# Performance work log

Hardware: AMD Instinct MI355X
Metric: run time of the kernel (lower is better)

The kernel has to match this reference:

```python
import jax, jax.numpy as jnp
import numpy as np

B, IN, H = 16384, 512, 1024

def setup_inputs() -> dict:
    key = jax.random.key(0)
    ks = jax.random.split(key, 9)
    s_h = 1.0 / np.sqrt(H)
    s_x = 1.0 / np.sqrt(IN)
    return {
        "x": jax.random.normal(ks[0], (B, IN), jnp.float32),
        "h_prev": jax.random.normal(ks[1], (B, H), jnp.float32),
        # SLIM1 gates: Linear(H->H, bias=True)
        "W_u": jax.random.uniform(ks[2], (H, H), jnp.float32, -s_h, s_h),
        "b_u": jax.random.uniform(ks[3], (H,), jnp.float32, -s_h, s_h),
        "W_r": jax.random.uniform(ks[4], (H, H), jnp.float32, -s_h, s_h),
        "b_r": jax.random.uniform(ks[5], (H,), jnp.float32, -s_h, s_h),
        # hidden candidate: Linear(IN->H, bias=False) and Linear(H->H, bias=True)
        "W_hx": jax.random.uniform(ks[6], (H, IN), jnp.float32, -s_x, s_x),
        "W_hh": jax.random.uniform(ks[7], (H, H), jnp.float32, -s_h, s_h),
        "b_h": jax.random.uniform(ks[8], (H,), jnp.float32, -s_h, s_h),
    }

def reference(x, h_prev, W_u, b_u, W_r, b_r, W_hx, W_hh, b_h):
    # update and reset gates depend only on h_prev (SLIM1: sigmoid(W h + b))
    u = jax.nn.sigmoid(h_prev @ W_u.T + b_u)          # [B, H]
    r = jax.nn.sigmoid(h_prev @ W_r.T + b_r)          # [B, H]
    # candidate hidden state: tanh(W_hx x + W_hh (r*h) + b)
    h_cand = jnp.tanh(x @ W_hx.T + (r * h_prev) @ W_hh.T + b_h)  # [B, H]
    h_next = (1.0 - u) * h_prev + u * h_cand
    return (h_next, h_next)
```

## Files before the change

kernel.cpp:

```cpp
#include <hip/hip_runtime.h>
#include <hip/hip_bf16.h>

#define M_DIM 16384
#define IN_DIM 512
#define H_DIM 1024
#define BH (M_DIM * H_DIM)
#define K2 1536

typedef float f32x4 __attribute__((ext_vector_type(4)));
typedef short bf16x8 __attribute__((ext_vector_type(8)));

static __device__ __forceinline__ unsigned short f2bf(float f) {
    union { float f; unsigned u; } a; a.f = f;
    unsigned r = a.u + 0x7fffu + ((a.u >> 16) & 1u);
    return (unsigned short)(r >> 16);
}
static __device__ __forceinline__ float bf2f(unsigned short u) {
    union { unsigned u; float f; } a; a.u = (unsigned)u << 16;
    return a.f;
}

#define OFF_HB   0u
#define OFF_A2   16777216u
#define OFF_WU   41943040u
#define OFF_WR   42991616u
#define OFF_W2   44040192u
#define OFF_U16  45613056u
#define WS2_ELEMS 62390272u
#define WS2_NEED_BYTES (WS2_ELEMS * 2ull)

__global__ __launch_bounds__(256) void k_conv(const float* __restrict__ x,
                                              const float* __restrict__ h,
                                              const float* __restrict__ wu,
                                              const float* __restrict__ whx,
                                              const float* __restrict__ whh,
                                              const float* __restrict__ wr,
                                              unsigned short* __restrict__ ws) {
    const int total = 3604480;
    for (int u = blockIdx.x * blockDim.x + threadIdx.x; u < total;
         u += gridDim.x * blockDim.x) {
        const float* src; unsigned short* d; int lu;
        if (u < 2097152)      { lu = u;
                                src = h + (size_t)lu * 8;
                                d = ws + OFF_HB + (size_t)lu * 8; }
        else if (u < 3145728) { lu = u - 2097152;
                                src = x + (size_t)lu * 8;
                                d = ws + OFF_A2 + (size_t)(lu >> 6) * K2 + (lu & 63) * 8; }
        else if (u < 3276800) { lu = u - 3145728;
                                src = wu + (size_t)lu * 8;
                                d = ws + OFF_WU + (size_t)lu * 8; }
        else if (u < 3342336) { lu = u - 3276800;
                                src = whx + (size_t)lu * 8;
                                d = ws + OFF_W2 + (size_t)(lu >> 6) * K2 + (lu & 63) * 8; }
        else if (u < 3473408) { lu = u - 3342336;
                                src = whh + (size_t)lu * 8;
                                d = ws + OFF_W2 + (size_t)(lu >> 7) * K2 + 512 + (lu & 127) * 8; }
        else                  { lu = u - 3473408;
                                src = wr + (size_t)lu * 8;
                                d = ws + OFF_WR + (size_t)lu * 8; }
        float4 a = *reinterpret_cast<const float4*>(src);
        float4 b = *reinterpret_cast<const float4*>(src + 4);
        uint4 p;
        p.x = (unsigned)f2bf(a.x) | ((unsigned)f2bf(a.y) << 16);
        p.y = (unsigned)f2bf(a.z) | ((unsigned)f2bf(a.w) << 16);
        p.z = (unsigned)f2bf(b.x) | ((unsigned)f2bf(b.y) << 16);
        p.w = (unsigned)f2bf(b.z) | ((unsigned)f2bf(b.w) << 16);
        *reinterpret_cast<uint4*>(d) = p;
    }
}

#define SLOT_E 24576

static __device__ __forceinline__ void stage_half512(const unsigned short* __restrict__ src,
                                                     int rowBase, int ld, int ks,
                                                     unsigned short* lds, int tid) {
#pragma unroll
    for (int i = 0; i < 2; ++i) {
        int c = i * 512 + tid;
        int r = c >> 3, kc = c & 7;
        int gc = kc ^ (r & 7);
        const unsigned short* g = src + (size_t)(rowBase + r) * ld + ks + gc * 8;
        __builtin_amdgcn_global_load_lds((const __attribute__((address_space(1))) void*)g,
                                         (__attribute__((address_space(3))) void*)(lds + c * 8),
                                         16, 0, 0);
    }
}

template <int NT>
static __device__ __forceinline__ void gemm_pipe(const unsigned short* __restrict__ A, int aLd,
                                                 const unsigned short* __restrict__ B, int bLd,
                                                 int bm, int bn, unsigned short* L,
                                                 int tid, int wm, int wn, int frow, int klane,
                                                 f32x4 acc[4][4]) {
    auto stage_unit = [&](int t, int u) {
        unsigned short* slot = L + (t % 3) * SLOT_E;
        if (u == 0)      stage_half512(A, bm * 256,       aLd, t * 64, slot,         tid);
        else if (u == 1) stage_half512(A, bm * 256 + 128, aLd, t * 64, slot + 8192,  tid);
        else             stage_half512(B, bn * 128,       bLd, t * 64, slot + 16384, tid);
    };

    stage_unit(0, 0); stage_unit(0, 1); stage_unit(0, 2);
    stage_unit(1, 0); stage_unit(1, 1); stage_unit(1, 2);
    asm volatile("s_waitcnt vmcnt(6)" ::: "memory");
    __builtin_amdgcn_s_barrier();

    for (int t = 0; t < NT; ++t) {
        const unsigned short* base  = L + (t % 3) * SLOT_E;
        const unsigned short* bbase = base + 16384;
        bf16x8 bv[4][2];
#pragma unroll
        for (int q = 0; q < 4; ++q) {
            if (q == 0) {
#pragma unroll
                for (int n = 0; n < 4; ++n)
#pragma unroll
                    for (int kk = 0; kk < 2; ++kk) {
                        int pr = wn * 64 + n * 16 + frow;
                        bv[n][kk] = *reinterpret_cast<const bf16x8*>(
                            &bbase[pr * 64 + (((kk << 2) + klane) ^ (pr & 7)) * 8]);
                    }
            }
            bf16x8 av[2];
#pragma unroll
            for (int kk = 0; kk < 2; ++kk) {
                int pr = wm * 64 + q * 16 + frow;
                av[kk] = *reinterpret_cast<const bf16x8*>(
                    &base[pr * 64 + (((kk << 2) + klane) ^ (pr & 7)) * 8]);
            }
            if (q < 3 && t + 2 < NT) stage_unit(t + 2, q);
            __builtin_amdgcn_s_barrier();
            __builtin_amdgcn_s_setprio(1);
#pragma unroll
            for (int kk = 0; kk < 2; ++kk)
#pragma unroll
                for (int n = 0; n < 4; ++n)
                    acc[q][n] = __builtin_amdgcn_mfma_f32_16x16x32_bf16(av[kk], bv[n][kk], acc[q][n], 0, 0, 0);
            __builtin_amdgcn_s_setprio(0);
            if (q < 3) __builtin_amdgcn_s_barrier();
        }
        if (t < NT - 2)       { asm volatile("s_waitcnt vmcnt(6)" ::: "memory"); }
        else if (t == NT - 2) { asm volatile("s_waitcnt vmcnt(0)" ::: "memory"); }
        __builtin_amdgcn_s_barrier();
    }
}

__global__ __launch_bounds__(512, 1) void k_rgate_s(const unsigned short* __restrict__ hb,
                                                    const unsigned short* __restrict__ wrb,
                                                    const float* __restrict__ b_r,
                                                    unsigned short* __restrict__ rhA2) {
    __shared__ unsigned short L[3 * SLOT_E];
    int bid = blockIdx.x;
    int swz = (bid & 7) * 64 + (bid >> 3);
    int bm = swz >> 3, bn = swz & 7;
    int tid = threadIdx.x;
    int wave = tid >> 6, lane = tid & 63;
    int wm = wave >> 1, wn = wave & 1;
    int frow = lane & 15, klane = lane >> 4;

    f32x4 acc[4][4] = {};
    gemm_pipe<16>(hb, H_DIM, wrb, H_DIM, bm, bn, L, tid, wm, wn, frow, klane, acc);

    int rbase = bm * 256 + wm * 64;
    int cbase = bn * 128 + wn * 64;
#pragma unroll
    for (int q = 0; q < 4; ++q) {
#pragma unroll
        for (int n = 0; n < 4; ++n) {
            int col = cbase + n * 16 + frow;
            float bs = b_r[col];
#pragma unroll
            for (int qq = 0; qq < 4; ++qq) {
                int row = rbase + q * 16 + klane * 4 + qq;
                float g = 1.0f / (1.0f + __expf(-(acc[q][n][qq] + bs)));
                rhA2[(size_t)row * K2 + col] = f2bf(g * bf2f(hb[(size_t)row * H_DIM + col]));
            }
        }
    }
}

__global__ __launch_bounds__(512, 1) void k_ugate_s(const unsigned short* __restrict__ hb,
                                                    const unsigned short* __restrict__ wub,
                                                    const float* __restrict__ b_u,
                                                    unsigned short* __restrict__ u16) {
    __shared__ unsigned short L[3 * SLOT_E];
    int bid = blockIdx.x;
    int swz = (bid & 7) * 64 + (bid >> 3);
    int bm = swz >> 3, bn = swz & 7;
    int tid = threadIdx.x;
    int wave = tid >> 6, lane = tid & 63;
    int wm = wave >> 1, wn = wave & 1;
    int frow = lane & 15, klane = lane >> 4;

    f32x4 acc[4][4] = {};
    gemm_pipe<16>(hb, H_DIM, wub, H_DIM, bm, bn, L, tid, wm, wn, frow, klane, acc);

    int rbase = bm * 256 + wm * 64;
    int cbase = bn * 128 + wn * 64;
#pragma unroll
    for (int q = 0; q < 4; ++q) {
#pragma unroll
        for (int n = 0; n < 4; ++n) {
            int col = cbase + n * 16 + frow;
            float bs = b_u[col];
#pragma unroll
            for (int qq = 0; qq < 4; ++qq) {
                int row = rbase + q * 16 + klane * 4 + qq;
                float g = 1.0f / (1.0f + __expf(-(acc[q][n][qq] + bs)));
                u16[(size_t)row * H_DIM + col] = f2bf(g);
            }
        }
    }
}

__global__ __launch_bounds__(512, 1) void k_cand_b(const unsigned short* __restrict__ a2,
                                                   const unsigned short* __restrict__ w2,
                                                   const unsigned short* __restrict__ hb,
                                                   const unsigned short* __restrict__ u16,
                                                   const float* __restrict__ b_h,
                                                   float* __restrict__ out) {
    __shared__ unsigned short L[3 * SLOT_E];
    int bid = blockIdx.x;
    int swz = (bid & 7) * 64 + (bid >> 3);
    int bm = swz >> 3, bn = swz & 7;
    int tid = threadIdx.x;
    int wave = tid >> 6, lane = tid & 63;
    int wm = wave >> 1, wn = wave & 1;
    int frow = lane & 15, klane = lane >> 4;

    f32x4 acc[4][4] = {};
    gemm_pipe<24>(a2, K2, w2, K2, bm, bn, L, tid, wm, wn, frow, klane, acc);

    int rbase = bm * 256 + wm * 64;
    int cbase = bn * 128 + wn * 64;
#pragma unroll
    for (int q = 0; q < 4; ++q) {
#pragma unroll
        for (int n = 0; n < 4; ++n) {
            int col = cbase + n * 16 + frow;
            float bh = b_h[col];
#pragma unroll
            for (int qq = 0; qq < 4; ++qq) {
                int row = rbase + q * 16 + klane * 4 + qq;
                size_t off = (size_t)row * H_DIM + col;
                float hp = bf2f(hb[off]);
                float u = bf2f(u16[off]);
                float cpre = acc[q][n][qq] + bh;
                cpre = fminf(fmaxf(cpre, -15.0f), 15.0f);
                float e = __expf(2.0f * cpre);
                float c = (e - 1.0f) / (e + 1.0f);
                float h = hp + u * (c - hp);
                out[off] = h;
                out[BH + off] = h;
            }
        }
    }
}

#define LDSS 40

static __device__ __forceinline__ void stage_f32(const float* __restrict__ src, int rowBase,
                                                 int ld, int kBase,
                                                 unsigned short* lds, int tid) {
#pragma unroll
    for (int i = 0; i < 4; ++i) {
        int idx = i * 256 + tid;
        int r = idx >> 3, c4 = idx & 7;
        const float4 v = *reinterpret_cast<const float4*>(
            src + (size_t)(rowBase + r) * ld + kBase + c4 * 4);
        uint2 p;
        p.x = (unsigned)f2bf(v.x) | ((unsigned)f2bf(v.y) << 16);
        p.y = (unsigned)f2bf(v.z) | ((unsigned)f2bf(v.w) << 16);
        *reinterpret_cast<uint2*>(lds + r * LDSS + c4 * 4) = p;
    }
}

static __device__ __forceinline__ void stage_bf16s(const unsigned short* __restrict__ src,
                                                   int rowBase, int ld, int kBase,
                                                   unsigned short* lds, int tid) {
#pragma unroll
    for (int i = 0; i < 2; ++i) {
        int idx = i * 256 + tid;
        int r = idx >> 2, c8 = idx & 3;
        const uint4 v = *reinterpret_cast<const uint4*>(
            src + (size_t)(rowBase + r) * ld + kBase + c8 * 8);
        *reinterpret_cast<uint4*>(lds + r * LDSS + c8 * 8) = v;
    }
}

__global__ __launch_bounds__(256, 2) void k_rgate(const float* __restrict__ h_prev,
                                                  const float* __restrict__ W_r,
                                                  const float* __restrict__ b_r,
                                                  unsigned short* __restrict__ rh) {
    __shared__ unsigned short As[128 * LDSS];
    __shared__ unsigned short Bs[128 * LDSS];
    int bid = blockIdx.x;
    int swz = (bid & 7) * 128 + (bid >> 3);
    int bm = swz >> 3, bn = swz & 7;
    int tid = threadIdx.x;
    int wave = tid >> 6, lane = tid & 63;
    int wm = wave >> 1, wn = wave & 1;
    int frow = lane & 15, koff = (lane >> 4) * 8;
    f32x4 acc[4][4] = {};
    for (int ks = 0; ks < H_DIM; ks += 32) {
        stage_f32(h_prev, bm * 128, H_DIM, ks, As, tid);
        stage_f32(W_r, bn * 128, H_DIM, ks, Bs, tid);
        __syncthreads();
        bf16x8 av[4], bv[4];
#pragma unroll
        for (int m = 0; m < 4; ++m)
            av[m] = *reinterpret_cast<const bf16x8*>(&As[(wm * 64 + m * 16 + frow) * LDSS + koff]);
#pragma unroll
        for (int n = 0; n < 4; ++n)
            bv[n] = *reinterpret_cast<const bf16x8*>(&Bs[(wn * 64 + n * 16 + frow) * LDSS + koff]);
#pragma unroll
        for (int m = 0; m < 4; ++m)
#pragma unroll
            for (int n = 0; n < 4; ++n)
                acc[m][n] = __builtin_amdgcn_mfma_f32_16x16x32_bf16(av[m], bv[n], acc[m][n], 0, 0, 0);
        __syncthreads();
    }
    int rbase = bm * 128 + wm * 64, cbase = bn * 128 + wn * 64;
#pragma unroll
    for (int m = 0; m < 4; ++m)
#pragma unroll
        for (int n = 0; n < 4; ++n) {
            int col = cbase + n * 16 + frow;
            float bias = b_r[col];
#pragma unroll
            for (int q = 0; q < 4; ++q) {
                int row = rbase + m * 16 + (lane >> 4) * 4 + q;
                float pre = acc[m][n][q] + bias;
                float rv = 1.0f / (1.0f + __expf(-pre));
                rh[(size_t)row * H_DIM + col] = f2bf(rv * h_prev[(size_t)row * H_DIM + col]);
            }
        }
}

__global__ __launch_bounds__(256, 2) void k_fused(const float* __restrict__ x,
                                                  const float* __restrict__ h_prev,
                                                  const float* __restrict__ W_u,
                                                  const float* __restrict__ b_u,
                                                  const float* __restrict__ W_hx,
                                                  const float* __restrict__ W_hh,
                                                  const float* __restrict__ b_h,
                                                  const unsigned short* __restrict__ rh,
                                                  float* __restrict__ out) {
    __shared__ unsigned short As[128 * LDSS];
    __shared__ unsigned short Bs[128 * LDSS];
    int bid = blockIdx.x;
    int swz = (bid & 7) * 128 + (bid >> 3);
    int bm = swz >> 3, bn = swz & 7;
    int tid = threadIdx.x;
    int wave = tid >> 6, lane = tid & 63;
    int wm = wave >> 1, wn = wave & 1;
    int frow = lane & 15, koff = (lane >> 4) * 8;
    f32x4 accu[4][4] = {};
    f32x4 accc[4][4] = {};
    for (int ks = 0; ks < H_DIM; ks += 32) {
        stage_f32(h_prev, bm * 128, H_DIM, ks, As, tid);
        stage_f32(W_u, bn * 128, H_DIM, ks, Bs, tid);
        __syncthreads();
        bf16x8 av[4], bv[4];
#pragma unroll
        for (int m = 0; m < 4; ++m)
            av[m] = *reinterpret_cast<const bf16x8*>(&As[(wm * 64 + m * 16 + frow) * LDSS + koff]);
#pragma unroll
        for (int n = 0; n < 4; ++n)
            bv[n] = *reinterpret_cast<const bf16x8*>(&Bs[(wn * 64 + n * 16 + frow) * LDSS + koff]);
#pragma unroll
        for (int m = 0; m < 4; ++m)
#pragma unroll
            for (int n = 0; n < 4; ++n)
                accu[m][n] = __builtin_amdgcn_mfma_f32_16x16x32_bf16(av[m], bv[n], accu[m][n], 0, 0, 0);
        __syncthreads();
    }
    for (int ks = 0; ks < IN_DIM; ks += 32) {
        stage_f32(x, bm * 128, IN_DIM, ks, As, tid);
        stage_f32(W_hx, bn * 128, IN_DIM, ks, Bs, tid);
        __syncthreads();
        bf16x8 av[4], bv[4];
#pragma unroll
        for (int m = 0; m < 4; ++m)
            av[m] = *reinterpret_cast<const bf16x8*>(&As[(wm * 64 + m * 16 + frow) * LDSS + koff]);
#pragma unroll
        for (int n = 0; n < 4; ++n)
            bv[n] = *reinterpret_cast<const bf16x8*>(&Bs[(wn * 64 + n * 16 + frow) * LDSS + koff]);
#pragma unroll
        for (int m = 0; m < 4; ++m)
#pragma unroll
            for (int n = 0; n < 4; ++n)
                accc[m][n] = __builtin_amdgcn_mfma_f32_16x16x32_bf16(av[m], bv[n], accc[m][n], 0, 0, 0);
        __syncthreads();
    }
    for (int ks = 0; ks < H_DIM; ks += 32) {
        stage_bf16s(rh, bm * 128, H_DIM, ks, As, tid);
        stage_f32(W_hh, bn * 128, H_DIM, ks, Bs, tid);
        __syncthreads();
        bf16x8 av[4], bv[4];
#pragma unroll
        for (int m = 0; m < 4; ++m)
            av[m] = *reinterpret_cast<const bf16x8*>(&As[(wm * 64 + m * 16 + frow) * LDSS + koff]);
#pragma unroll
        for (int n = 0; n < 4; ++n)
            bv[n] = *reinterpret_cast<const bf16x8*>(&Bs[(wn * 64 + n * 16 + frow) * LDSS + koff]);
#pragma unroll
        for (int m = 0; m < 4; ++m)
#pragma unroll
            for (int n = 0; n < 4; ++n)
                accc[m][n] = __builtin_amdgcn_mfma_f32_16x16x32_bf16(av[m], bv[n], accc[m][n], 0, 0, 0);
        __syncthreads();
    }
    int rbase = bm * 128 + wm * 64, cbase = bn * 128 + wn * 64;
#pragma unroll
    for (int m = 0; m < 4; ++m)
#pragma unroll
        for (int n = 0; n < 4; ++n) {
            int col = cbase + n * 16 + frow;
            float bu = b_u[col], bh = b_h[col];
#pragma unroll
            for (int q = 0; q < 4; ++q) {
                int row = rbase + m * 16 + (lane >> 4) * 4 + q;
                size_t off = (size_t)row * H_DIM + col;
                float hp = h_prev[off];
                float u = 1.0f / (1.0f + __expf(-(accu[m][n][q] + bu)));
                float cpre = accc[m][n][q] + bh;
                cpre = fminf(fmaxf(cpre, -15.0f), 15.0f);
                float e = __expf(2.0f * cpre);
                float c = (e - 1.0f) / (e + 1.0f);
                float h = hp + u * (c - hp);
                out[off] = h;
                out[BH + off] = h;
            }
        }
}

extern "C" void kernel_launch(void* const* d_in, const int* in_sizes, int n_in,
                              void* d_out, int out_size, void* d_ws, size_t ws_size,
                              hipStream_t stream) {
    const float* x      = (const float*)d_in[0];
    const float* h_prev = (const float*)d_in[1];
    const float* W_u    = (const float*)d_in[2];
    const float* b_u    = (const float*)d_in[3];
    const float* W_r    = (const float*)d_in[4];
    const float* b_r    = (const float*)d_in[5];
    const float* W_hx   = (const float*)d_in[6];
    const float* W_hh   = (const float*)d_in[7];
    const float* b_h    = (const float*)d_in[8];
    float* out = (float*)d_out;

    if (ws_size >= WS2_NEED_BYTES) {
        unsigned short* ws = (unsigned short*)d_ws;
        hipLaunchKernelGGL(k_conv, dim3(2048), dim3(256), 0, stream,
                           x, h_prev, W_u, W_hx, W_hh, W_r, ws);
        hipLaunchKernelGGL(k_rgate_s, dim3(512), dim3(512), 0, stream,
                           ws + OFF_HB, ws + OFF_WR, b_r, ws + OFF_A2 + 512);
        hipLaunchKernelGGL(k_ugate_s, dim3(512), dim3(512), 0, stream,
                           ws + OFF_HB, ws + OFF_WU, b_u, ws + OFF_U16);
        hipLaunchKernelGGL(k_cand_b, dim3(512), dim3(512), 0, stream,
                           ws + OFF_A2, ws + OFF_W2, ws + OFF_HB, ws + OFF_U16,
                           b_h, out);
    } else {
        unsigned short* rh = (unsigned short*)d_ws;
        hipLaunchKernelGGL(k_rgate, dim3(1024), dim3(256), 0, stream, h_prev, W_r, b_r, rh);
        hipLaunchKernelGGL(k_fused, dim3(1024), dim3(256), 0, stream,
                           x, h_prev, W_u, b_u, W_hx, W_hh, b_h, rh, out);
    }
}
```

Baseline: 209.9 us.

## Switch bf16 GEMMs to 256x256 tiles with double-buffered quadrant pipeline

Replaces the 256x128 block tile with a triple-buffered LDS pipeline by a 256x256 tile, with 8 waves in a 2x4 layout each holding a 128x64 accumulator. Staging is double-buffered and split into A/B halves that are prefetched between four MFMA quadrant phases. The grid is halved to 256 blocks for all three GEMM kernels. The aim is more arithmetic per byte loaded from global memory and LDS. In exchange, register pressure doubles for the accumulators, and with 256 blocks on a 256-CU part there is only one wave of work, so any imbalance is not hidden.

Result: no change. 207.2 us (-1.3%).

```diff
diff --git a/kernel.cpp b/kernel.cpp
--- a/kernel.cpp
+++ b/kernel.cpp
@@ -69,109 +69,130 @@
     }
 }
 
-#define SLOT_E 24576
-
-static __device__ __forceinline__ void stage_half512(const unsigned short* __restrict__ src,
-                                                     int rowBase, int ld, int ks,
-                                                     unsigned short* lds, int tid) {
-#pragma unroll
-    for (int i = 0; i < 2; ++i) {
-        int c = i * 512 + tid;
-        int r = c >> 3, kc = c & 7;
-        int gc = kc ^ (r & 7);
-        const unsigned short* g = src + (size_t)(rowBase + r) * ld + ks + gc * 8;
-        __builtin_amdgcn_global_load_lds((const __attribute__((address_space(1))) void*)g,
-                                         (__attribute__((address_space(3))) void*)(lds + c * 8),
-                                         16, 0, 0);
-    }
-}
-
 template <int NT>
-static __device__ __forceinline__ void gemm_pipe(const unsigned short* __restrict__ A, int aLd,
-                                                 const unsigned short* __restrict__ B, int bLd,
-                                                 int bm, int bn, unsigned short* L,
-                                                 int tid, int wm, int wn, int frow, int klane,
-                                                 f32x4 acc[4][4]) {
-    auto stage_unit = [&](int t, int u) {
-        unsigned short* slot = L + (t % 3) * SLOT_E;
-        if (u == 0)      stage_half512(A, bm * 256,       aLd, t * 64, slot,         tid);
-        else if (u == 1) stage_half512(A, bm * 256 + 128, aLd, t * 64, slot + 8192,  tid);
-        else             stage_half512(B, bn * 128,       bLd, t * 64, slot + 16384, tid);
+static __device__ __forceinline__ void gemm_256(const unsigned short* __restrict__ A, int aLd,
+                                                const unsigned short* __restrict__ B, int bLd,
+                                                int bm, int bn, unsigned short* L, int tid,
+                                                int wm, int wn, int frow, int klane,
+                                                f32x4 acc[8][4]) {
+    auto stA = [&](int t, int mh) {
+#pragma unroll
+        for (int i = 0; i < 2; ++i) {
+            int c = i * 512 + tid;
+            int rp = c >> 3, kc = c & 7;
+            int gc = kc ^ (rp & 7);
+            int grow = bm * 256 + mh * 64 + (rp & 63) + ((rp >> 6) << 7);
+            const unsigned short* g = A + (size_t)grow * aLd + t * 64 + gc * 8;
+            unsigned short* l = L + (t & 1) * 32768 + mh * 8192 + c * 8;
+            __builtin_amdgcn_global_load_lds((const __attribute__((address_space(1))) void*)g,
+                                             (__attribute__((address_space(3))) void*)l, 16, 0, 0);
+        }
     };
-
-    stage_unit(0, 0); stage_unit(0, 1); stage_unit(0, 2);
-    stage_unit(1, 0); stage_unit(1, 1); stage_unit(1, 2);
-    asm volatile("s_waitcnt vmcnt(6)" ::: "memory");
+    auto stB = [&](int t, int nh) {
+#pragma unroll
+        for (int i = 0; i < 2; ++i) {
+            int c = i * 512 + tid;
+            int rp = c >> 3, kc = c & 7;
+            int gc = kc ^ (rp & 7);
+            int grow = bn * 256 + nh * 32 + (rp & 31) + ((rp >> 5) << 6);
+            const unsigned short* g = B + (size_t)grow * bLd + t * 64 + gc * 8;
+            unsigned short* l = L + (t & 1) * 32768 + 16384 + nh * 8192 + c * 8;
+            __builtin_amdgcn_global_load_lds((const __attribute__((address_space(1))) void*)g,
+                                             (__attribute__((address_space(3))) void*)l, 16, 0, 0);
+        }
+    };
+
+    stA(0, 0); stA(0, 1); stB(0, 0); stB(0, 1);
+    stA(1, 0); stB(1, 0);
+    asm volatile("s_waitcnt vmcnt(4)" ::: "memory");
     __builtin_amdgcn_s_barrier();
 
-    for (int t = 0; t < NT; ++t) {
-        const unsigned short* base  = L + (t % 3) * SLOT_E;
-        const unsigned short* bbase = base + 16384;
-        bf16x8 bv[4][2];
-#pragma unroll
-        for (int q = 0; q < 4; ++q) {
-            if (q == 0) {
-#pragma unroll
-                for (int n = 0; n < 4; ++n)
-#pragma unroll
-                    for (int kk = 0; kk < 2; ++kk) {
-                        int pr = wn * 64 + n * 16 + frow;
-                        bv[n][kk] = *reinterpret_cast<const bf16x8*>(
-                            &bbase[pr * 64 + (((kk << 2) + klane) ^ (pr & 7)) * 8]);
-                    }
-            }
-            bf16x8 av[2];
-#pragma unroll
-            for (int kk = 0; kk < 2; ++kk) {
-                int pr = wm * 64 + q * 16 + frow;
-                av[kk] = *reinterpret_cast<const bf16x8*>(
-                    &base[pr * 64 + (((kk << 2) + klane) ^ (pr & 7)) * 8]);
-            }
-            if (q < 3 && t + 2 < NT) stage_unit(t + 2, q);
-            __builtin_amdgcn_s_barrier();
-            __builtin_amdgcn_s_setprio(1);
-#pragma unroll
-            for (int kk = 0; kk < 2; ++kk)
-#pragma unroll
-                for (int n = 0; n < 4; ++n)
-                    acc[q][n] = __builtin_amdgcn_mfma_f32_16x16x32_bf16(av[kk], bv[n][kk], acc[q][n], 0, 0, 0);
-            __builtin_amdgcn_s_setprio(0);
-            if (q < 3) __builtin_amdgcn_s_barrier();
-        }
-        if (t < NT - 2)       { asm volatile("s_waitcnt vmcnt(6)" ::: "memory"); }
-        else if (t == NT - 2) { asm volatile("s_waitcnt vmcnt(0)" ::: "memory"); }
-        __builtin_amdgcn_s_barrier();
-    }
+#define LOAD_AV(mh)                                                                  \
+    _Pragma("unroll") for (int mf = 0; mf < 4; ++mf)                                 \
+        _Pragma("unroll") for (int kk = 0; kk < 2; ++kk) {                           \
+            int rp = wm * 64 + mf * 16 + frow;                                       \
+            av[mf][kk] = *reinterpret_cast<const bf16x8*>(                           \
+                &Lb[(mh) * 8192 + rp * 64 + (((kk << 2) + klane) ^ (rp & 7)) * 8]);  \
+        }
+#define LOAD_BV(nh)                                                                  \
+    _Pragma("unroll") for (int nf = 0; nf < 2; ++nf)                                 \
+        _Pragma("unroll") for (int kk = 0; kk < 2; ++kk) {                           \
+            int rp = wn * 32 + nf * 16 + frow;                                       \
+            bv[nf][kk] = *reinterpret_cast<const bf16x8*>(                           \
+                &LbB[(nh) * 8192 + rp * 64 + (((kk << 2) + klane) ^ (rp & 7)) * 8]); \
+        }
+#define MFMA_Q(mbase, nbase)                                                         \
+    __builtin_amdgcn_s_setprio(1);                                                   \
+    _Pragma("unroll") for (int kk = 0; kk < 2; ++kk)                                 \
+        _Pragma("unroll") for (int mf = 0; mf < 4; ++mf)                             \
+            _Pragma("unroll") for (int nf = 0; nf < 2; ++nf)                         \
+                acc[(mbase) + mf][(nbase) + nf] =                                    \
+                    __builtin_amdgcn_mfma_f32_16x16x32_bf16(                         \
+                        av[mf][kk], bv[nf][kk], acc[(mbase) + mf][(nbase) + nf],     \
+                        0, 0, 0);                                                    \
+    __builtin_amdgcn_s_setprio(0);
+
+    for (int g = 0; g < NT; ++g) {
+        const unsigned short* Lb = L + (g & 1) * 32768;
+        const unsigned short* LbB = Lb + 16384;
+        bf16x8 av[4][2], bv[2][2];
+
+        LOAD_AV(0); LOAD_BV(0);
+        if (g + 1 < NT) stA(g + 1, 1);
+        __builtin_amdgcn_s_barrier();
+        MFMA_Q(0, 0);
+        __builtin_amdgcn_s_barrier();
+        LOAD_BV(1);
+        if (g + 1 < NT) stB(g + 1, 1);
+        __builtin_amdgcn_s_barrier();
+        MFMA_Q(0, 2);
+        __builtin_amdgcn_s_barrier();
+        LOAD_AV(1); LOAD_BV(0);
+        if (g + 2 < NT) stA(g + 2, 0);
+        __builtin_amdgcn_s_barrier();
+        MFMA_Q(4, 0);
+        __builtin_amdgcn_s_barrier();
+        LOAD_BV(1);
+        if (g + 2 < NT) stB(g + 2, 0);
+        __builtin_amdgcn_s_barrier();
+        MFMA_Q(4, 2);
+        if (g < NT - 2)       { asm volatile("s_waitcnt vmcnt(4)" ::: "memory"); }
+        else if (g == NT - 2) { asm volatile("s_waitcnt vmcnt(0)" ::: "memory"); }
+        __builtin_amdgcn_s_barrier();
+    }
+#undef LOAD_AV
+#undef LOAD_BV
+#undef MFMA_Q
 }
 
 __global__ __launch_bounds__(512, 1) void k_rgate_s(const unsigned short* __restrict__ hb,
                                                     const unsigned short* __restrict__ wrb,
                                                     const float* __restrict__ b_r,
                                                     unsigned short* __restrict__ rhA2) {
-    __shared__ unsigned short L[3 * SLOT_E];
+    __shared__ unsigned short L[65536];
     int bid = blockIdx.x;
-    int swz = (bid & 7) * 64 + (bid >> 3);
-    int bm = swz >> 3, bn = swz & 7;
+    int swz = (bid & 7) * 32 + (bid >> 3);
+    int bm = swz >> 2, bn = swz & 3;
     int tid = threadIdx.x;
     int wave = tid >> 6, lane = tid & 63;
-    int wm = wave >> 1, wn = wave & 1;
+    int wm = wave >> 2, wn = wave & 3;
     int frow = lane & 15, klane = lane >> 4;
 
-    f32x4 acc[4][4] = {};
-    gemm_pipe<16>(hb, H_DIM, wrb, H_DIM, bm, bn, L, tid, wm, wn, frow, klane, acc);
-
-    int rbase = bm * 256 + wm * 64;
-    int cbase = bn * 128 + wn * 64;
-#pragma unroll
-    for (int q = 0; q < 4; ++q) {
-#pragma unroll
-        for (int n = 0; n < 4; ++n) {
-            int col = cbase + n * 16 + frow;
+    f32x4 acc[8][4] = {};
+    gemm_256<16>(hb, H_DIM, wrb, H_DIM, bm, bn, L, tid, wm, wn, frow, klane, acc);
+
+    int rbase = bm * 256 + wm * 128;
+    int cbase = bn * 256 + wn * 64;
+#pragma unroll
+    for (int a = 0; a < 8; ++a) {
+#pragma unroll
+        for (int nn = 0; nn < 4; ++nn) {
+            int col = cbase + nn * 16 + frow;
             float bs = b_r[col];
 #pragma unroll
-            for (int qq = 0; qq < 4; ++qq) {
-                int row = rbase + q * 16 + klane * 4 + qq;
-                float g = 1.0f / (1.0f + __expf(-(acc[q][n][qq] + bs)));
+            for (int q = 0; q < 4; ++q) {
+                int row = rbase + a * 16 + klane * 4 + q;
+                float g = 1.0f / (1.0f + __expf(-(acc[a][nn][q] + bs)));
                 rhA2[(size_t)row * K2 + col] = f2bf(g * bf2f(hb[(size_t)row * H_DIM + col]));
             }
         }
@@ -182,30 +203,30 @@
                                                     const unsigned short* __restrict__ wub,
                                                     const float* __restrict__ b_u,
                                                     unsigned short* __restrict__ u16) {
-    __shared__ unsigned short L[3 * SLOT_E];
+    __shared__ unsigned short L[65536];
     int bid = blockIdx.x;
-    int swz = (bid & 7) * 64 + (bid >> 3);
-    int bm = swz >> 3, bn = swz & 7;
+    int swz = (bid & 7) * 32 + (bid >> 3);
+    int bm = swz >> 2, bn = swz & 3;
     int tid = threadIdx.x;
     int wave = tid >> 6, lane = tid & 63;
-    int wm = wave >> 1, wn = wave & 1;
+    int wm = wave >> 2, wn = wave & 3;
     int frow = lane & 15, klane = lane >> 4;
 
-    f32x4 acc[4][4] = {};
-    gemm_pipe<16>(hb, H_DIM, wub, H_DIM, bm, bn, L, tid, wm, wn, frow, klane, acc);
-
-    int rbase = bm * 256 + wm * 64;
-    int cbase = bn * 128 + wn * 64;
-#pragma unroll
-    for (int q = 0; q < 4; ++q) {
-#pragma unroll
-        for (int n = 0; n < 4; ++n) {
-            int col = cbase + n * 16 + frow;
+    f32x4 acc[8][4] = {};
+    gemm_256<16>(hb, H_DIM, wub, H_DIM, bm, bn, L, tid, wm, wn, frow, klane, acc);
+
+    int rbase = bm * 256 + wm * 128;
+    int cbase = bn * 256 + wn * 64;
+#pragma unroll
+    for (int a = 0; a < 8; ++a) {
+#pragma unroll
+        for (int nn = 0; nn < 4; ++nn) {
+            int col = cbase + nn * 16 + frow;
             float bs = b_u[col];
 #pragma unroll
-            for (int qq = 0; qq < 4; ++qq) {
-                int row = rbase + q * 16 + klane * 4 + qq;
-                float g = 1.0f / (1.0f + __expf(-(acc[q][n][qq] + bs)));
+            for (int q = 0; q < 4; ++q) {
+                int row = rbase + a * 16 + klane * 4 + q;
+                float g = 1.0f / (1.0f + __expf(-(acc[a][nn][q] + bs)));
                 u16[(size_t)row * H_DIM + col] = f2bf(g);
             }
         }
@@ -218,33 +239,33 @@
                                                    const unsigned short* __restrict__ u16,
                                                    const float* __restrict__ b_h,
                                                    float* __restrict__ out) {
-    __shared__ unsigned short L[3 * SLOT_E];
+    __shared__ unsigned short L[65536];
     int bid = blockIdx.x;
-    int swz = (bid & 7) * 64 + (bid >> 3);
-    int bm = swz >> 3, bn = swz & 7;
+    int swz = (bid & 7) * 32 + (bid >> 3);
+    int bm = swz >> 2, bn = swz & 3;
     int tid = threadIdx.x;
     int wave = tid >> 6, lane = tid & 63;
-    int wm = wave >> 1, wn = wave & 1;
+    int wm = wave >> 2, wn = wave & 3;
     int frow = lane & 15, klane = lane >> 4;
 
-    f32x4 acc[4][4] = {};
-    gemm_pipe<24>(a2, K2, w2, K2, bm, bn, L, tid, wm, wn, frow, klane, acc);
-
-    int rbase = bm * 256 + wm * 64;
-    int cbase = bn * 128 + wn * 64;
-#pragma unroll
-    for (int q = 0; q < 4; ++q) {
-#pragma unroll
-        for (int n = 0; n < 4; ++n) {
-            int col = cbase + n * 16 + frow;
+    f32x4 acc[8][4] = {};
+    gemm_256<24>(a2, K2, w2, K2, bm, bn, L, tid, wm, wn, frow, klane, acc);
+
+    int rbase = bm * 256 + wm * 128;
+    int cbase = bn * 256 + wn * 64;
+#pragma unroll
+    for (int a = 0; a < 8; ++a) {
+#pragma unroll
+        for (int nn = 0; nn < 4; ++nn) {
+            int col = cbase + nn * 16 + frow;
             float bh = b_h[col];
 #pragma unroll
-            for (int qq = 0; qq < 4; ++qq) {
-                int row = rbase + q * 16 + klane * 4 + qq;
+            for (int q = 0; q < 4; ++q) {
+                int row = rbase + a * 16 + klane * 4 + q;
                 size_t off = (size_t)row * H_DIM + col;
                 float hp = bf2f(hb[off]);
                 float u = bf2f(u16[off]);
-                float cpre = acc[q][n][qq] + bh;
+                float cpre = acc[a][nn][q] + bh;
                 cpre = fminf(fmaxf(cpre, -15.0f), 15.0f);
                 float e = __expf(2.0f * cpre);
                 float c = (e - 1.0f) / (e + 1.0f);
@@ -452,11 +473,11 @@
         unsigned short* ws = (unsigned short*)d_ws;
         hipLaunchKernelGGL(k_conv, dim3(2048), dim3(256), 0, stream,
                            x, h_prev, W_u, W_hx, W_hh, W_r, ws);
-        hipLaunchKernelGGL(k_rgate_s, dim3(512), dim3(512), 0, stream,
+        hipLaunchKernelGGL(k_rgate_s, dim3(256), dim3(512), 0, stream,
                            ws + OFF_HB, ws + OFF_WR, b_r, ws + OFF_A2 + 512);
-        hipLaunchKernelGGL(k_ugate_s, dim3(512), dim3(512), 0, stream,
+        hipLaunchKernelGGL(k_ugate_s, dim3(256), dim3(512), 0, stream,
                            ws + OFF_HB, ws + OFF_WU, b_u, ws + OFF_U16);
-        hipLaunchKernelGGL(k_cand_b, dim3(512), dim3(512), 0, stream,
+        hipLaunchKernelGGL(k_cand_b, dim3(256), dim3(512), 0, stream,
                            ws + OFF_A2, ws + OFF_W2, ws + OFF_HB, ws + OFF_U16,
                            b_h, out);
     } else {
```
